# Kernel optimization log

Hardware: AMD Instinct MI355X
Metric: run time of the kernel (lower is better)

## Reference

```python
import jax, jax.numpy as jnp
import numpy as np

HEADS = 8   # from init_kwargs
K_SIZE = 64

def setup_inputs() -> dict:
    key = jax.random.key(0)
    k1, k2, k3, k4 = jax.random.split(key, 4)
    B, C, D = 4, 2048, 1024
    return {
        "x": jax.random.normal(k1, (B, C, D), dtype=jnp.float32),
        "Mq": jax.random.normal(k2, (D, HEADS * K_SIZE), dtype=jnp.float32) * 0.02,
        "Mk": jax.random.normal(k3, (D, HEADS * K_SIZE), dtype=jnp.float32) * 0.02,
        "Mv": jax.random.normal(k4, (D, 1024), dtype=jnp.float32) * 0.02,
    }

def reference(x, Mq, Mk, Mv):
    B, C, _ = x.shape
    H, K = HEADS, K_SIZE
    V = Mv.shape[1] // H  # v_size = output_size // heads = 128
    # Faithful to torch: (x @ M).view(B, H, C, -1) is a raw row-major reshape
    # of the [B, C, H*K] projection, which mixes token and head axes exactly
    # as the original module does.
    q = (x @ Mq).reshape(B, H, C, K)
    k = (x @ Mk).reshape(B, H, C, K)
    v = (x @ Mv).reshape(B, H, C, V)
    # scores: [B*H, C, C]; scale by sqrt(k_size); softmax over dim=1 (the
    # first C axis), matching the original's unusual softmax dim.
    scores = jnp.einsum('bhqk,bhck->bhqc', q, k).reshape(B * H, C, C)
    att = jax.nn.softmax(scores / jnp.sqrt(jnp.float32(K)), axis=1)
    # att_weights.view(B, C, heads, -1): raw reshape from [B*H, C, C]
    att4 = att.reshape(B, C, H, C)
    # intended semantics of `att4 @ v`: per-head attn-weighted sum of values
    out = jnp.einsum('bqhc,bhcd->bqhd', att4, v)  # [B, C, H, V]
    return out.reshape(B, C, H * V)
```

## Files before the change

### kernel.cpp

```cpp
#include <hip/hip_runtime.h>
#include <stdint.h>
#include <stddef.h>


typedef short     bf8v  __attribute__((ext_vector_type(8)));
typedef float     f4v   __attribute__((ext_vector_type(4)));
typedef unsigned short u16x4 __attribute__((ext_vector_type(4)));
typedef unsigned short u16x8 __attribute__((ext_vector_type(8)));

__device__ __forceinline__ unsigned short f2bf(float f) {
    union { float f; uint32_t u; } v; v.f = f;
    return (unsigned short)((v.u + 0x7fffu + ((v.u >> 16) & 1u)) >> 16);
}

#define MFMA32(A, B, C) __builtin_amdgcn_mfma_f32_16x16x32_bf16((A), (B), (C), 0, 0, 0)

__global__ __launch_bounds__(256) void k_cvt(const float* __restrict__ in,
                                             unsigned short* __restrict__ out, int n4) {
    int i = blockIdx.x * 256 + threadIdx.x;
    if (i >= n4) return;
    f4v v = *(const f4v*)(in + (size_t)i * 4);
    u16x4 o;
    o[0] = f2bf(v[0]); o[1] = f2bf(v[1]); o[2] = f2bf(v[2]); o[3] = f2bf(v[3]);
    *(u16x4*)(out + (size_t)i * 4) = o;
}

__global__ __launch_bounds__(256) void k_cvtT3(const float* __restrict__ Mq,
                                               const float* __restrict__ Mk,
                                               const float* __restrict__ Mv,
                                               unsigned short* __restrict__ wqt,
                                               unsigned short* __restrict__ wkt,
                                               unsigned short* __restrict__ wvt) {
    __shared__ unsigned short t[64][68];
    const int tid = threadIdx.x;
    const int tr = tid >> 4, tc4 = (tid & 15) * 4;
    const float* in; unsigned short* outT; int Ncols, cb;
    if (blockIdx.z == 0) {
        if (blockIdx.x < 8) { in = Mq; outT = wqt; Ncols = 512; cb = blockIdx.x * 64; }
        else                { in = Mk; outT = wkt; Ncols = 512; cb = (blockIdx.x - 8) * 64; }
    } else                  { in = Mv; outT = wvt; Ncols = 1024; cb = blockIdx.x * 64; }
    const int rb = blockIdx.y * 64;
#pragma unroll
    for (int p = 0; p < 4; ++p) {
        int r = tr + p * 16;
        f4v v = *(const f4v*)(in + (size_t)(rb + r) * Ncols + cb + tc4);
        t[r][tc4 + 0] = f2bf(v[0]); t[r][tc4 + 1] = f2bf(v[1]);
        t[r][tc4 + 2] = f2bf(v[2]); t[r][tc4 + 3] = f2bf(v[3]);
    }
    __syncthreads();
#pragma unroll
    for (int p = 0; p < 4; ++p) {
        int r = tr + p * 16;
        u16x4 o;
        o[0] = t[tc4 + 0][r]; o[1] = t[tc4 + 1][r];
        o[2] = t[tc4 + 2][r]; o[3] = t[tc4 + 3][r];
        *(u16x4*)(outT + (size_t)(cb + r) * 1024 + rb + tc4) = o;
    }
}

__global__ __launch_bounds__(256) void k_T(const unsigned short* __restrict__ in,
                                           unsigned short* __restrict__ out) {
    __shared__ unsigned short t[64][68];
    const int tid = threadIdx.x;
    const int tr = tid >> 4, tc4 = (tid & 15) * 4;
    const int rb = blockIdx.y * 64, cb = blockIdx.x * 64;
    const unsigned short* ib = in  + (size_t)blockIdx.z * 262144;
    unsigned short*       ob = out + (size_t)blockIdx.z * 262144;
#pragma unroll
    for (int p = 0; p < 4; ++p) {
        int r = tr + p * 16;
        u16x4 v = *(const u16x4*)(ib + (size_t)(rb + r) * 128 + cb + tc4);
        t[r][tc4 + 0] = v[0]; t[r][tc4 + 1] = v[1];
        t[r][tc4 + 2] = v[2]; t[r][tc4 + 3] = v[3];
    }
    __syncthreads();
#pragma unroll
    for (int p = 0; p < 4; ++p) {
        int r = tr + p * 16;
        u16x4 o;
        o[0] = t[tc4 + 0][r]; o[1] = t[tc4 + 1][r];
        o[2] = t[tc4 + 2][r]; o[3] = t[tc4 + 3][r];
        *(u16x4*)(ob + (size_t)(cb + r) * 2048 + rb + tc4) = o;
    }
}

__global__ __launch_bounds__(256, 2) void k_gemm(const unsigned short* __restrict__ X,
                                                 const unsigned short* __restrict__ Wt,
                                                 unsigned short* __restrict__ pq,
                                                 unsigned short* __restrict__ pk,
                                                 unsigned short* __restrict__ pv) {
    __shared__ __align__(16) unsigned short xs[128][72];
    __shared__ __align__(16) unsigned short wls[128][72];
    const int tid = threadIdx.x;
    const int lane = tid & 63, w = tid >> 6;
    const int lc = lane & 15, quad = lane >> 4;
    const int rowb = blockIdx.x * 128, cb = blockIdx.y;

    unsigned short* outp; int N, colb;
    if (cb < 4)      { outp = pq; N = 512;  colb = cb * 128; }
    else if (cb < 8) { outp = pk; N = 512;  colb = (cb - 4) * 128; }
    else             { outp = pv; N = 1024; colb = (cb - 8) * 128; }

    f4v acc[2][8];
#pragma unroll
    for (int mt = 0; mt < 2; ++mt)
#pragma unroll
        for (int nt = 0; nt < 8; ++nt) acc[mt][nt] = f4v{0.f, 0.f, 0.f, 0.f};

    for (int k0 = 0; k0 < 1024; k0 += 64) {
#pragma unroll
        for (int p = 0; p < 4; ++p) {
            int v = tid + p * 256;
            int r = v >> 3, s = (v & 7) * 8;
            *(u16x8*)(&xs[r][s])  = *(const u16x8*)(X  + (size_t)(rowb + r) * 1024 + k0 + s);
            *(u16x8*)(&wls[r][s]) = *(const u16x8*)(Wt + (size_t)(cb * 128 + r) * 1024 + k0 + s);
        }
        __syncthreads();
#pragma unroll
        for (int ks = 0; ks < 2; ++ks) {
            int kk = ks * 32 + quad * 8;
            bf8v bx[8];
#pragma unroll
            for (int nt = 0; nt < 8; ++nt) bx[nt] = *(const bf8v*)(&xs[nt * 16 + lc][kk]);
#pragma unroll
            for (int mt = 0; mt < 2; ++mt) {
                bf8v a = *(const bf8v*)(&wls[w * 32 + mt * 16 + lc][kk]);
#pragma unroll
                for (int nt = 0; nt < 8; ++nt) acc[mt][nt] = MFMA32(a, bx[nt], acc[mt][nt]);
            }
        }
        __syncthreads();
    }
#pragma unroll
    for (int mt = 0; mt < 2; ++mt)
#pragma unroll
        for (int nt = 0; nt < 8; ++nt) {
            int crow = rowb + nt * 16 + lc;
            int ccol = colb + w * 32 + mt * 16 + quad * 4;
            u16x4 o;
            o[0] = f2bf(acc[mt][nt][0]); o[1] = f2bf(acc[mt][nt][1]);
            o[2] = f2bf(acc[mt][nt][2]); o[3] = f2bf(acc[mt][nt][3]);
            *(u16x4*)(outp + (size_t)crow * N + ccol) = o;
        }
}

__global__ __launch_bounds__(256, 2) void k_pass1(const unsigned short* __restrict__ Pq,
                                                  const unsigned short* __restrict__ Pk,
                                                  float* __restrict__ rdenl) {
    __shared__ __align__(16) unsigned short qs[128][72];
    __shared__ __align__(16) unsigned short kss[128][72];
    __shared__ float dsum[4][128];
    const int tid = threadIdx.x;
    const int lane = tid & 63, w = tid >> 6;
    const int lc = lane & 15, quad = lane >> 4;
    const int c2b = blockIdx.x * 128;
    const int bg  = blockIdx.y;
    const unsigned short* qbase = Pq + (size_t)bg * 131072;
    const unsigned short* kbase = Pk + (size_t)bg * 131072 + (size_t)c2b * 64;

#pragma unroll
    for (int p = 0; p < 4; ++p) {
        int v = tid + p * 256;
        int r = v >> 3, s = (v & 7) * 8;
        *(u16x8*)(&kss[r][s]) = *(const u16x8*)(kbase + (size_t)v * 8);
    }

    float csum[8];
#pragma unroll
    for (int nt = 0; nt < 8; ++nt) csum[nt] = 0.f;

    for (int it = 0; it < 16; ++it) {
        __syncthreads();
        const unsigned short* qit = qbase + (size_t)it * 8192;
#pragma unroll
        for (int p = 0; p < 4; ++p) {
            int v = tid + p * 256;
            int r = v >> 3, s = (v & 7) * 8;
            *(u16x8*)(&qs[r][s]) = *(const u16x8*)(qit + (size_t)v * 8);
        }
        __syncthreads();

        f4v sc[2][8];
#pragma unroll
        for (int mt = 0; mt < 2; ++mt)
#pragma unroll
            for (int nt = 0; nt < 8; ++nt) sc[mt][nt] = f4v{0.f, 0.f, 0.f, 0.f};
#pragma unroll
        for (int ks = 0; ks < 2; ++ks) {
            int kk = ks * 32 + quad * 8;
            bf8v bk[8];
#pragma unroll
            for (int nt = 0; nt < 8; ++nt) bk[nt] = *(const bf8v*)(&kss[nt * 16 + lc][kk]);
#pragma unroll
            for (int mt = 0; mt < 2; ++mt) {
                bf8v a = *(const bf8v*)(&qs[w * 32 + mt * 16 + lc][kk]);
#pragma unroll
                for (int nt = 0; nt < 8; ++nt) sc[mt][nt] = MFMA32(a, bk[nt], sc[mt][nt]);
            }
        }
#pragma unroll
        for (int mt = 0; mt < 2; ++mt)
#pragma unroll
            for (int nt = 0; nt < 8; ++nt)
#pragma unroll
                for (int r = 0; r < 4; ++r)
                    csum[nt] += __expf(sc[mt][nt][r] * 0.125f);
    }

#pragma unroll
    for (int nt = 0; nt < 8; ++nt) {
        float v = csum[nt];
        v += __shfl_xor(v, 16, 64);
        v += __shfl_xor(v, 32, 64);
        if (quad == 0) dsum[w][nt * 16 + lc] = v;
    }
    __syncthreads();
    if (tid < 128) {
        float tot = dsum[0][tid] + dsum[1][tid] + dsum[2][tid] + dsum[3][tid];
        rdenl[(size_t)bg * 2048 + c2b + tid] = -__logf(tot);
    }
}

__global__ __launch_bounds__(256, 2) void k_pass2(const unsigned short* __restrict__ Pq,
                                                  const unsigned short* __restrict__ Pk,
                                                  const unsigned short* __restrict__ Vt,
                                                  const float* __restrict__ rdenl,
                                                  float* __restrict__ out) {
    __shared__ __align__(16) unsigned short qs[128][72];
    __shared__ __align__(16) unsigned short kss[2][64][72];
    __shared__ __align__(16) unsigned short vs[2][128][72];
    const int tid = threadIdx.x;
    const int lane = tid & 63, w = tid >> 6;
    const int lc = lane & 15, quad = lane >> 4;
    const int jt = blockIdx.x, h = blockIdx.y, bg = blockIdx.z;
    const int b = bg >> 3, g = bg & 7;

    const unsigned short* qbase = Pq + (size_t)bg * 131072;
    const unsigned short* kbase = Pk + (size_t)bg * 131072;
    const unsigned short* vbase = Vt + (size_t)(b * 8 + h) * 262144;
    const float* rdl = rdenl + (size_t)bg * 2048;

#pragma unroll
    for (int p = 0; p < 4; ++p) {
        int v = tid + p * 256;
        int i = v >> 3, s = (v & 7) * 8;
        *(u16x8*)(&qs[i][s]) =
            *(const u16x8*)(qbase + (size_t)((jt * 128 + i) * 8 + h) * 64 + s);
    }
#pragma unroll
    for (int p = 0; p < 2; ++p) {
        int v = tid + p * 256;
        int c8 = ((v & 7) + (v >> 6)) & 7;
        *(u16x8*)(&kss[0][v >> 3][c8 * 8]) = *(const u16x8*)(kbase + (size_t)v * 8);
    }
#pragma unroll
    for (int p = 0; p < 4; ++p) {
        int v = tid + p * 256;
        int d = v >> 3, s = (v & 7) * 8;
        *(u16x8*)(&vs[0][d][s]) = *(const u16x8*)(vbase + (size_t)d * 2048 + s);
    }
    __syncthreads();

    bf8v bq[2][2];
#pragma unroll
    for (int nt = 0; nt < 2; ++nt)
#pragma unroll
        for (int ks = 0; ks < 2; ++ks)
            bq[nt][ks] = *(const bf8v*)(&qs[w * 32 + nt * 16 + lc][ks * 32 + quad * 8]);

    f4v acc[8][2];
#pragma unroll
    for (int dt = 0; dt < 8; ++dt)
#pragma unroll
        for (int nt = 0; nt < 2; ++nt) acc[dt][nt] = f4v{0.f, 0.f, 0.f, 0.f};

    for (int cc = 0; cc < 32; ++cc) {
        const int buf = cc & 1;
        u16x8 kreg[2], vreg[4];
        if (cc < 31) {
            const int c2n = (cc + 1) * 64;
#pragma unroll
            for (int p = 0; p < 2; ++p) {
                int v = tid + p * 256;
                kreg[p] = *(const u16x8*)(kbase + (size_t)c2n * 64 + (size_t)v * 8);
            }
#pragma unroll
            for (int p = 0; p < 4; ++p) {
                int v = tid + p * 256;
                vreg[p] = *(const u16x8*)(vbase + (size_t)(v >> 3) * 2048 + c2n + (v & 7) * 8);
            }
        }

        f4v sc[4][2];
#pragma unroll
        for (int mt = 0; mt < 4; ++mt)
#pragma unroll
            for (int nt = 0; nt < 2; ++nt) sc[mt][nt] = f4v{0.f, 0.f, 0.f, 0.f};
#pragma unroll
        for (int ks = 0; ks < 2; ++ks) {
            bf8v a[4];
#pragma unroll
            for (int mt = 0; mt < 4; ++mt) {
                int rlog = ((mt >> 1) << 5) + ((lc >> 2) << 3) + ((mt & 1) << 2) + (lc & 3);
                int c8   = ((ks << 2) + quad + ((mt >> 1) << 2) + (lc >> 2)) & 7;
                a[mt] = *(const bf8v*)(&kss[buf][rlog][c8 * 8]);
            }
#pragma unroll
            for (int mt = 0; mt < 4; ++mt)
#pragma unroll
                for (int nt = 0; nt < 2; ++nt)
                    sc[mt][nt] = MFMA32(a[mt], bq[nt][ks], sc[mt][nt]);
        }

        bf8v pb[2][2];
#pragma unroll
        for (int mt = 0; mt < 4; ++mt) {
            f4v lrd = *(const f4v*)(rdl + cc * 64 + ((mt >> 1) << 5) + (quad << 3) + ((mt & 1) << 2));
#pragma unroll
            for (int nt = 0; nt < 2; ++nt)
#pragma unroll
                for (int i = 0; i < 4; ++i)
                    pb[mt >> 1][nt][(mt & 1) * 4 + i] =
                        (short)f2bf(__expf(__builtin_fmaf(sc[mt][nt][i], 0.125f, lrd[i])));
        }

#pragma unroll
        for (int kc = 0; kc < 2; ++kc)
#pragma unroll
            for (int dt = 0; dt < 8; ++dt) {
                bf8v a = *(const bf8v*)(&vs[buf][dt * 16 + lc][kc * 32 + quad * 8]);
#pragma unroll
                for (int nt = 0; nt < 2; ++nt)
                    acc[dt][nt] = MFMA32(a, pb[kc][nt], acc[dt][nt]);
            }

        if (cc < 31) {
            const int nbuf = buf ^ 1;
#pragma unroll
            for (int p = 0; p < 2; ++p) {
                int v = tid + p * 256;
                int c8 = ((v & 7) + (v >> 6)) & 7;
                *(u16x8*)(&kss[nbuf][v >> 3][c8 * 8]) = kreg[p];
            }
#pragma unroll
            for (int p = 0; p < 4; ++p) {
                int v = tid + p * 256;
                *(u16x8*)(&vs[nbuf][v >> 3][(v & 7) * 8]) = vreg[p];
            }
        }
        __syncthreads();
    }

    float* ob = out + (size_t)(b * 2048 + g * 256 + jt * 128) * 1024 + h * 128;
#pragma unroll
    for (int dt = 0; dt < 8; ++dt)
#pragma unroll
        for (int nt = 0; nt < 2; ++nt) {
            int r = w * 32 + nt * 16 + lc;
            int d = dt * 16 + quad * 4;
            *(f4v*)(ob + (size_t)r * 1024 + d) = acc[dt][nt];
        }
}

extern "C" void kernel_launch(void* const* d_in, const int* in_sizes, int n_in,
                              void* d_out, int out_size, void* d_ws, size_t ws_size,
                              hipStream_t stream) {
    const float* x  = (const float*)d_in[0];
    const float* Mq = (const float*)d_in[1];
    const float* Mk = (const float*)d_in[2];
    const float* Mv = (const float*)d_in[3];
    float* out = (float*)d_out;

    char* base = (char*)d_ws;
    unsigned short* xb  = (unsigned short*)base;  base += 16777216;
    unsigned short* wqt = (unsigned short*)base;  base += 1048576;
    unsigned short* wkt = (unsigned short*)base;  base += 1048576;
    unsigned short* wvt = (unsigned short*)base;  base += 2097152;
    unsigned short* pq  = (unsigned short*)base;  base += 8388608;
    unsigned short* pk  = (unsigned short*)base;  base += 8388608;
    unsigned short* pv  = (unsigned short*)base;  base += 16777216;
    unsigned short* vt  = (unsigned short*)base;  base += 16777216;
    float* rdenl = (float*)base;                  base += 262144;

    k_cvt<<<8192, 256, 0, stream>>>(x, xb, 2097152);
    k_cvtT3<<<dim3(16, 16, 2), 256, 0, stream>>>(Mq, Mk, Mv, wqt, wkt, wvt);
    k_gemm<<<dim3(64, 16), 256, 0, stream>>>(xb, wqt , pq, pk, pv);
    k_T<<<dim3(2, 32, 32), 256, 0, stream>>>(pv, vt);
    k_pass1<<<dim3(16, 32), 256, 0, stream>>>(pq, pk, rdenl);
    k_pass2<<<dim3(2, 8, 32), 256, 0, stream>>>(pq, pk, vt, rdenl, out);
}
```

Before: 254.2 us.

## Double-buffer GEMM and pass1 tiles with async global-to-LDS loads and XOR swizzle

The projection GEMM and the softmax-denominator pass now load tiles with global_load_lds straight into double-buffered shared memory. The next tile is prefetched while MFMAs run on the current one, and the rows use an XOR swizzle in place of padding to avoid LDS bank conflicts. The 1/sqrt(K) scale is folded into the Q projection epilogue, which removes the per-score multiply in pass1 and pass2. This costs extra LDS per block, which may reduce occupancy. With a single barrier per iteration, correctness depends on the async load having completed at that barrier.

Result: faster. 230.4 us (-9.4%).

```diff
diff --git a/kernel.cpp b/kernel.cpp
--- a/kernel.cpp
+++ b/kernel.cpp
@@ -14,6 +14,9 @@
 }
 
 #define MFMA32(A, B, C) __builtin_amdgcn_mfma_f32_16x16x32_bf16((A), (B), (C), 0, 0, 0)
+#define ASYNC16(g, l) __builtin_amdgcn_global_load_lds(                        \
+    (const __attribute__((address_space(1))) unsigned int*)(g),                \
+    (__attribute__((address_space(3))) unsigned int*)(l), 16, 0, 0)
 
 __global__ __launch_bounds__(256) void k_cvt(const float* __restrict__ in,
                                              unsigned short* __restrict__ out, int n4) {
@@ -89,17 +92,20 @@
                                                  unsigned short* __restrict__ pq,
                                                  unsigned short* __restrict__ pk,
                                                  unsigned short* __restrict__ pv) {
-    __shared__ __align__(16) unsigned short xs[128][72];
-    __shared__ __align__(16) unsigned short wls[128][72];
+    __shared__ __align__(16) unsigned short xs[2][8192];
+    __shared__ __align__(16) unsigned short ws2[2][8192];
     const int tid = threadIdx.x;
     const int lane = tid & 63, w = tid >> 6;
     const int lc = lane & 15, quad = lane >> 4;
     const int rowb = blockIdx.x * 128, cb = blockIdx.y;
 
-    unsigned short* outp; int N, colb;
-    if (cb < 4)      { outp = pq; N = 512;  colb = cb * 128; }
-    else if (cb < 8) { outp = pk; N = 512;  colb = (cb - 4) * 128; }
-    else             { outp = pv; N = 1024; colb = (cb - 8) * 128; }
+    unsigned short* outp; int N, colb; float scale;
+    if (cb < 4)      { outp = pq; N = 512;  colb = cb * 128;       scale = 0.125f; }
+    else if (cb < 8) { outp = pk; N = 512;  colb = (cb - 4) * 128; scale = 1.0f; }
+    else             { outp = pv; N = 1024; colb = (cb - 8) * 128; scale = 1.0f; }
+
+    const int lr   = lane >> 3;
+    const int swz  = ((lane & 7) ^ lr) * 8;
 
     f4v acc[2][8];
 #pragma unroll
@@ -107,24 +113,39 @@
 #pragma unroll
         for (int nt = 0; nt < 8; ++nt) acc[mt][nt] = f4v{0.f, 0.f, 0.f, 0.f};
 
-    for (int k0 = 0; k0 < 1024; k0 += 64) {
-#pragma unroll
-        for (int p = 0; p < 4; ++p) {
-            int v = tid + p * 256;
-            int r = v >> 3, s = (v & 7) * 8;
-            *(u16x8*)(&xs[r][s])  = *(const u16x8*)(X  + (size_t)(rowb + r) * 1024 + k0 + s);
-            *(u16x8*)(&wls[r][s]) = *(const u16x8*)(Wt + (size_t)(cb * 128 + r) * 1024 + k0 + s);
-        }
-        __syncthreads();
+#pragma unroll
+    for (int j = 0; j < 4; ++j) {
+        int row = (w * 4 + j) * 8 + lr;
+        ASYNC16(X  + (size_t)(rowb + row) * 1024 + swz,            &xs[0][(w * 4 + j) * 512]);
+        ASYNC16(Wt + (size_t)(cb * 128 + row) * 1024 + swz,        &ws2[0][(w * 4 + j) * 512]);
+    }
+    __syncthreads();
+
+    for (int k = 0; k < 16; ++k) {
+        const int buf = k & 1;
+        if (k < 15) {
+            const int k0n = (k + 1) * 64;
+#pragma unroll
+            for (int j = 0; j < 4; ++j) {
+                int row = (w * 4 + j) * 8 + lr;
+                ASYNC16(X  + (size_t)(rowb + row) * 1024 + k0n + swz,     &xs[buf ^ 1][(w * 4 + j) * 512]);
+                ASYNC16(Wt + (size_t)(cb * 128 + row) * 1024 + k0n + swz, &ws2[buf ^ 1][(w * 4 + j) * 512]);
+            }
+        }
 #pragma unroll
         for (int ks = 0; ks < 2; ++ks) {
-            int kk = ks * 32 + quad * 8;
             bf8v bx[8];
 #pragma unroll
-            for (int nt = 0; nt < 8; ++nt) bx[nt] = *(const bf8v*)(&xs[nt * 16 + lc][kk]);
+            for (int nt = 0; nt < 8; ++nt) {
+                int row = nt * 16 + lc;
+                int c8  = (ks * 4 + quad) ^ (lc & 7);
+                bx[nt] = *(const bf8v*)(&xs[buf][row * 64 + c8 * 8]);
+            }
 #pragma unroll
             for (int mt = 0; mt < 2; ++mt) {
-                bf8v a = *(const bf8v*)(&wls[w * 32 + mt * 16 + lc][kk]);
+                int row = w * 32 + mt * 16 + lc;
+                int c8  = (ks * 4 + quad) ^ (lc & 7);
+                bf8v a = *(const bf8v*)(&ws2[buf][row * 64 + c8 * 8]);
 #pragma unroll
                 for (int nt = 0; nt < 8; ++nt) acc[mt][nt] = MFMA32(a, bx[nt], acc[mt][nt]);
             }
@@ -138,8 +159,8 @@
             int crow = rowb + nt * 16 + lc;
             int ccol = colb + w * 32 + mt * 16 + quad * 4;
             u16x4 o;
-            o[0] = f2bf(acc[mt][nt][0]); o[1] = f2bf(acc[mt][nt][1]);
-            o[2] = f2bf(acc[mt][nt][2]); o[3] = f2bf(acc[mt][nt][3]);
+            o[0] = f2bf(acc[mt][nt][0] * scale); o[1] = f2bf(acc[mt][nt][1] * scale);
+            o[2] = f2bf(acc[mt][nt][2] * scale); o[3] = f2bf(acc[mt][nt][3] * scale);
             *(u16x4*)(outp + (size_t)crow * N + ccol) = o;
         }
 }
@@ -147,8 +168,8 @@
 __global__ __launch_bounds__(256, 2) void k_pass1(const unsigned short* __restrict__ Pq,
                                                   const unsigned short* __restrict__ Pk,
                                                   float* __restrict__ rdenl) {
-    __shared__ __align__(16) unsigned short qs[128][72];
-    __shared__ __align__(16) unsigned short kss[128][72];
+    __shared__ __align__(16) unsigned short kls[8192];
+    __shared__ __align__(16) unsigned short qls[2][8192];
     __shared__ float dsum[4][128];
     const int tid = threadIdx.x;
     const int lane = tid & 63, w = tid >> 6;
@@ -158,53 +179,63 @@
     const unsigned short* qbase = Pq + (size_t)bg * 131072;
     const unsigned short* kbase = Pk + (size_t)bg * 131072 + (size_t)c2b * 64;
 
-#pragma unroll
-    for (int p = 0; p < 4; ++p) {
-        int v = tid + p * 256;
-        int r = v >> 3, s = (v & 7) * 8;
-        *(u16x8*)(&kss[r][s]) = *(const u16x8*)(kbase + (size_t)v * 8);
-    }
+    const int lr  = lane >> 3;
+    const int swz = ((lane & 7) ^ lr) * 8;
+
+#pragma unroll
+    for (int j = 0; j < 4; ++j) {
+        int row = (w * 4 + j) * 8 + lr;
+        ASYNC16(kbase + (size_t)row * 64 + swz, &kls[(w * 4 + j) * 512]);
+        ASYNC16(qbase + (size_t)row * 64 + swz, &qls[0][(w * 4 + j) * 512]);
+    }
+    __syncthreads();
 
     float csum[8];
 #pragma unroll
     for (int nt = 0; nt < 8; ++nt) csum[nt] = 0.f;
 
     for (int it = 0; it < 16; ++it) {
+        const int buf = it & 1;
+        if (it < 15) {
+            const unsigned short* qn = qbase + (size_t)(it + 1) * 8192;
+#pragma unroll
+            for (int j = 0; j < 4; ++j) {
+                int row = (w * 4 + j) * 8 + lr;
+                ASYNC16(qn + (size_t)row * 64 + swz, &qls[buf ^ 1][(w * 4 + j) * 512]);
+            }
+        }
+
+        f4v sc[2][8];
+#pragma unroll
+        for (int mt = 0; mt < 2; ++mt)
+#pragma unroll
+            for (int nt = 0; nt < 8; ++nt) sc[mt][nt] = f4v{0.f, 0.f, 0.f, 0.f};
+#pragma unroll
+        for (int ks = 0; ks < 2; ++ks) {
+            bf8v bk[8];
+#pragma unroll
+            for (int nt = 0; nt < 8; ++nt) {
+                int row = nt * 16 + lc;
+                int c8  = (ks * 4 + quad) ^ (lc & 7);
+                bk[nt] = *(const bf8v*)(&kls[row * 64 + c8 * 8]);
+            }
+#pragma unroll
+            for (int mt = 0; mt < 2; ++mt) {
+                int row = w * 32 + mt * 16 + lc;
+                int c8  = (ks * 4 + quad) ^ (lc & 7);
+                bf8v a = *(const bf8v*)(&qls[buf][row * 64 + c8 * 8]);
+#pragma unroll
+                for (int nt = 0; nt < 8; ++nt) sc[mt][nt] = MFMA32(a, bk[nt], sc[mt][nt]);
+            }
+        }
+#pragma unroll
+        for (int mt = 0; mt < 2; ++mt)
+#pragma unroll
+            for (int nt = 0; nt < 8; ++nt)
+#pragma unroll
+                for (int r = 0; r < 4; ++r)
+                    csum[nt] += __expf(sc[mt][nt][r]);
         __syncthreads();
-        const unsigned short* qit = qbase + (size_t)it * 8192;
-#pragma unroll
-        for (int p = 0; p < 4; ++p) {
-            int v = tid + p * 256;
-            int r = v >> 3, s = (v & 7) * 8;
-            *(u16x8*)(&qs[r][s]) = *(const u16x8*)(qit + (size_t)v * 8);
-        }
-        __syncthreads();
-
-        f4v sc[2][8];
-#pragma unroll
-        for (int mt = 0; mt < 2; ++mt)
-#pragma unroll
-            for (int nt = 0; nt < 8; ++nt) sc[mt][nt] = f4v{0.f, 0.f, 0.f, 0.f};
-#pragma unroll
-        for (int ks = 0; ks < 2; ++ks) {
-            int kk = ks * 32 + quad * 8;
-            bf8v bk[8];
-#pragma unroll
-            for (int nt = 0; nt < 8; ++nt) bk[nt] = *(const bf8v*)(&kss[nt * 16 + lc][kk]);
-#pragma unroll
-            for (int mt = 0; mt < 2; ++mt) {
-                bf8v a = *(const bf8v*)(&qs[w * 32 + mt * 16 + lc][kk]);
-#pragma unroll
-                for (int nt = 0; nt < 8; ++nt) sc[mt][nt] = MFMA32(a, bk[nt], sc[mt][nt]);
-            }
-        }
-#pragma unroll
-        for (int mt = 0; mt < 2; ++mt)
-#pragma unroll
-            for (int nt = 0; nt < 8; ++nt)
-#pragma unroll
-                for (int r = 0; r < 4; ++r)
-                    csum[nt] += __expf(sc[mt][nt][r] * 0.125f);
     }
 
 #pragma unroll
@@ -321,7 +352,7 @@
 #pragma unroll
                 for (int i = 0; i < 4; ++i)
                     pb[mt >> 1][nt][(mt & 1) * 4 + i] =
-                        (short)f2bf(__expf(__builtin_fmaf(sc[mt][nt][i], 0.125f, lrd[i])));
+                        (short)f2bf(__expf(sc[mt][nt][i] + lrd[i]));
         }
 
 #pragma unroll
```
